# Kernel tuning notes

Hardware: AMD Instinct MI355X
Metric: run time of the kernel (lower is better)

The kernel has to match this reference:

```python
import jax, jax.numpy as jnp
import numpy as np

# hyperparams matching init_kwargs
T_LEN = 1024
T_LATENCY = 7
TB = T_LATENCY + 1          # t_len_block
N_OUT = 1024
BATCH = 32
FS_SCALE = 10.0             # FastSigmoid default scale


@jax.custom_vjp
def fast_sigmoid(x):
    # forward: Heaviside; backward: fast-sigmoid surrogate
    return (x > 0).astype(x.dtype)

def _fs_fwd(x):
    return (x > 0).astype(x.dtype), x

def _fs_bwd(x, g):
    return (g / (FS_SCALE * jnp.abs(x) + 1.0) ** 2,)

fast_sigmoid.defvjp(_fs_fwd, _fs_bwd)


def setup_inputs() -> dict:
    key = jax.random.key(0)
    k1, k2, k3, k4 = jax.random.split(key, 4)
    x = jax.random.normal(k1, (T_LEN, BATCH, N_OUT), dtype=jnp.float32) * 0.6
    # raw params; forward applies the clamp/abs 'properties' of the module
    beta_raw = jax.random.uniform(k2, (N_OUT,), minval=0.7, maxval=0.99, dtype=jnp.float32)
    p_raw = jax.random.uniform(k3, (N_OUT,), minval=0.5, maxval=0.95, dtype=jnp.float32)
    b_raw = jax.random.uniform(k4, (N_OUT,), minval=0.2, maxval=1.0, dtype=jnp.float32)
    return {"x": x, "beta_raw": beta_raw, "p_raw": p_raw, "b_raw": b_raw}


def reference(x, beta_raw, p_raw, b_raw):
    T, B, N = x.shape
    tb = TB
    n_blocks = T // tb  # t_pad == 0 by construction
    dt = x.dtype

    # clamped properties
    beta = jnp.clip(beta_raw, 0.001, 0.999)          # [N]
    p = jnp.clip(jnp.abs(p_raw), 0.0, 0.999)         # [N]
    bb = jnp.clip(jnp.abs(b_raw), 0.001, 1.0)        # [N]

    t_idx = jnp.arange(tb)
    expo = t_idx[:, None] - t_idx[None, :]            # [tb,tb], t - s
    lower = expo >= 0
    # causal decay kernel: beta^(t-s) for s<=t  (grouped conv1d equivalent)
    beta_pow = jnp.where(lower[:, :, None],
                         beta[None, None, :] ** jnp.maximum(expo, 0)[:, :, None].astype(dt),
                         jnp.zeros((), dt))           # [tb,tb,N]
    # phi kernel: weight (t-s+1) for s<=t  (conv2d equivalent)
    phi = jnp.where(lower, (expo + 1).astype(dt), jnp.zeros((), dt))  # [tb,tb]
    p_exp = jnp.arange(1, tb + 1, dtype=dt)           # [tb]
    p_pow = p[None, :] ** p_exp[:, None]              # [tb,N]
    inv_p = 1.0 / p                                   # [N]

    def body(carry, x_slice):
        spikes, z, int_mem, a_kernel = carry          # [tb,B,N],[tb,B,N],[B,N],[tb,B,N]
        sg = jax.lax.stop_gradient(spikes)            # detach_spike_grad=True
        maskf = (jnp.max(sg, axis=0) > 0).astype(dt)  # [B,N] any spike in prev block
        # refractory masking of input
        xs = jnp.where(z < maskf[None], jnp.zeros((), dt), x_slice)
        v_init = int_mem * (1.0 - maskf)
        # adaptation update
        a_at_spike = jnp.sum(a_kernel * sg, axis=0) + inv_p          # [B,N]
        decay_steps = jnp.sum(z > 1, axis=0).astype(dt)              # [B,N]
        new_a = a_at_spike * jnp.power(p[None, :], decay_steps)
        a = a_kernel[-1] * (1.0 - maskf) + new_a * maskf             # [B,N]
        a_k = p_pow[:, None, :] * a[None]                             # [tb,B,N]
        v_th = 1.0 + bb[None, None, :] * a_k                          # [tb,B,N]
        # --- Block forward ---
        cur = xs.at[0].add(beta[None, :] * v_init)
        membrane = jnp.einsum('tsn,sbn->tbn', beta_pow, cur)          # causal decayed sum
        faulty = fast_sigmoid(membrane - v_th)                        # [tb,B,N] 0/1
        z_new = jnp.einsum('ts,sbn->tbn', phi, faulty)
        # g(): keep only entries exactly 1, straight-through grad
        spikes_new = z_new - jax.lax.stop_gradient(
            jnp.where(z_new == 1.0, jnp.zeros((), dt), z_new))
        return (spikes_new, z_new, membrane[-1], a_k), spikes_new

    z0 = jnp.zeros((tb, B, N), dt)
    carry0 = (z0, z0, jnp.zeros((B, N), dt), z0)
    xb = x.reshape(n_blocks, tb, B, N)
    _, out = jax.lax.scan(body, carry0, xb)
    return out.reshape(T, B, N)
```

## Files before the change

### kernel.cpp

```cpp
#include <hip/hip_runtime.h>


constexpr int T_LEN = 1024;
constexpr int TB    = 8;
constexpr int NBLK  = T_LEN / TB;
constexpr int BATCH = 32;
constexpr int NOUT  = 1024;
constexpr int BN    = BATCH * NOUT;
constexpr int PF    = 8;

__global__ __launch_bounds__(64, 1)
void snn_blocks_kernel(const float* __restrict__ x,
                       const float* __restrict__ beta_raw,
                       const float* __restrict__ p_raw,
                       const float* __restrict__ b_raw,
                       float* __restrict__ out)
{
    const int gid = blockIdx.x * 64 + threadIdx.x;
    const int n   = gid & (NOUT - 1);

    double beta = (double)beta_raw[n];
    beta = beta < 0.001 ? 0.001 : (beta > 0.999 ? 0.999 : beta);
    double p = fabs((double)p_raw[n]);
    p = p > 0.999 ? 0.999 : p;
    double bb = fabs((double)b_raw[n]);
    bb = bb < 0.001 ? 0.001 : (bb > 1.0 ? 1.0 : bb);
    const double inv_p = 1.0 / p;

    double ppow[9];
    ppow[0] = 1.0;
#pragma unroll
    for (int i = 1; i <= 8; ++i) ppow[i] = ppow[i - 1] * p;

    double bbp[8];
#pragma unroll
    for (int t = 0; t < 8; ++t) bbp[t] = bb * ppow[t + 1];

    double m = 0.0;
    double a = 0.0;
    int zprev[8];
#pragma unroll
    for (int t = 0; t < 8; ++t) zprev[t] = 0;

    const float* xg = x + gid;
    float*       og = out + gid;

    float xb[PF][8];
#pragma unroll
    for (int k = 0; k < PF; ++k) {
#pragma unroll
        for (int t = 0; t < 8; ++t)
            xb[k][t] = xg[(ptrdiff_t)(k * TB + t) * BN];
    }

#pragma unroll 8
    for (int blk = 0; blk < NBLK; ++blk) {
        const int slot = blk & (PF - 1);
        float cur[8];
#pragma unroll
        for (int t = 0; t < 8; ++t) cur[t] = xb[slot][t];

        const int pfb = blk + PF;
        if (pfb < NBLK) {
#pragma unroll
            for (int t = 0; t < 8; ++t)
                xb[slot][t] = xg[(ptrdiff_t)(pfb * TB + t) * BN];
        }

        int maskf = 0;
        int decay = 0;
        double ssum = 0.0;
#pragma unroll
        for (int t = 0; t < 8; ++t) {
            maskf |= (zprev[t] == 1);
            decay += (zprev[t] > 1) ? 1 : 0;
            ssum  += (zprev[t] == 1) ? ppow[t + 1] : 0.0;
        }

        const double a_at = a * ssum + inv_p;
        double pd = 1.0;
        pd *= (decay & 1) ? p       : 1.0;
        pd *= (decay & 2) ? ppow[2] : 1.0;
        pd *= (decay & 4) ? ppow[4] : 1.0;
        pd *= (decay & 8) ? ppow[8] : 1.0;
        const double new_a = a_at * pd;

        if (maskf) { a = new_a;      m = 0.0; }
        else       { a = ppow[8] * a;          }

        int c = 0, zc = 0;
        float* o = og + (ptrdiff_t)blk * TB * BN;
#pragma unroll
        for (int t = 0; t < 8; ++t) {
            double xv = (double)cur[t];
            if (maskf && zprev[t] == 0) xv = 0.0;
            m = beta * m + xv;
            const double vth = 1.0 + bbp[t] * a;
            const int f = (m - vth > 0.0) ? 1 : 0;
            c  += f;
            zc += c;
            zprev[t] = zc;
            __builtin_nontemporal_store((zc == 1) ? 1.0f : 0.0f,
                                        o + (ptrdiff_t)t * BN);
        }
    }
}

extern "C" void kernel_launch(void* const* d_in, const int* in_sizes, int n_in,
                              void* d_out, int out_size, void* d_ws, size_t ws_size,
                              hipStream_t stream) {
    const float* x        = (const float*)d_in[0];
    const float* beta_raw = (const float*)d_in[1];
    const float* p_raw    = (const float*)d_in[2];
    const float* b_raw    = (const float*)d_in[3];
    float* out            = (float*)d_out;

    dim3 grid(BN / 64);
    dim3 block(64);
    snn_blocks_kernel<<<grid, block, 0, stream>>>(x, beta_raw, p_raw, b_raw, out);
}
```

Measured before the change: 248.6 us.

## Prefetch input blocks via global_load_lds into LDS ring buffer with vmcnt waits

Replaces the register-held 8-block prefetch with direct global-to-LDS async loads into a 5-slot LDS ring, with prefetch depth 4 and explicit s_waitcnt vmcnt throttling. It also precomputes the next block's spike-mask summary (maskf, decay, ssum, zero bitmask) inside the time loop, so the zprev array is no longer kept. The aim is to free VGPRs and keep memory loads in flight without holding them in registers. The hand-tuned vmcnt counts depend on the nontemporal stores also counting toward vmcnt, so a wrong count could cause stale reads or extra stalls.

```diff
diff --git a/kernel.cpp b/kernel.cpp
--- a/kernel.cpp
+++ b/kernel.cpp
@@ -7,7 +7,13 @@
 constexpr int BATCH = 32;
 constexpr int NOUT  = 1024;
 constexpr int BN    = BATCH * NOUT;
-constexpr int PF    = 8;
+constexpr int PF    = 4;
+constexpr int SLOTS = 5;
+
+#define WAITVM(N) asm volatile("s_waitcnt vmcnt(" #N ")" ::: "memory")
+
+typedef const __attribute__((address_space(1))) void* gptr_t;
+typedef __attribute__((address_space(3))) void*       sptr_t;
 
 __global__ __launch_bounds__(64, 1)
 void snn_blocks_kernel(const float* __restrict__ x,
@@ -16,8 +22,11 @@
                        const float* __restrict__ b_raw,
                        float* __restrict__ out)
 {
-    const int gid = blockIdx.x * 64 + threadIdx.x;
-    const int n   = gid & (NOUT - 1);
+    __shared__ float lds[SLOTS][TB][64];
+
+    const int lane = threadIdx.x;
+    const int gid  = blockIdx.x * 64 + lane;
+    const int n    = gid & (NOUT - 1);
 
     double beta = (double)beta_raw[n];
     beta = beta < 0.001 ? 0.001 : (beta > 0.999 ? 0.999 : beta);
@@ -38,44 +47,31 @@
 
     double m = 0.0;
     double a = 0.0;
-    int zprev[8];
-#pragma unroll
-    for (int t = 0; t < 8; ++t) zprev[t] = 0;
+    int    maskf = 0;
+    int    decay = 0;
+    double ssum  = 0.0;
+    int    zzero = 0xFF;
 
     const float* xg = x + gid;
     float*       og = out + gid;
 
-    float xb[PF][8];
 #pragma unroll
     for (int k = 0; k < PF; ++k) {
 #pragma unroll
-        for (int t = 0; t < 8; ++t)
-            xb[k][t] = xg[(ptrdiff_t)(k * TB + t) * BN];
+        for (int t = 0; t < TB; ++t) {
+            __builtin_amdgcn_global_load_lds(
+                (gptr_t)(xg + (ptrdiff_t)(k * TB + t) * BN),
+                (sptr_t)&lds[k][t][0], 4, 0, 0);
+        }
     }
 
-#pragma unroll 8
-    for (int blk = 0; blk < NBLK; ++blk) {
-        const int slot = blk & (PF - 1);
+    int rs = 0;
+    int ws = PF % SLOTS;
+
+    auto body = [&](int blk) {
         float cur[8];
 #pragma unroll
-        for (int t = 0; t < 8; ++t) cur[t] = xb[slot][t];
-
-        const int pfb = blk + PF;
-        if (pfb < NBLK) {
-#pragma unroll
-            for (int t = 0; t < 8; ++t)
-                xb[slot][t] = xg[(ptrdiff_t)(pfb * TB + t) * BN];
-        }
-
-        int maskf = 0;
-        int decay = 0;
-        double ssum = 0.0;
-#pragma unroll
-        for (int t = 0; t < 8; ++t) {
-            maskf |= (zprev[t] == 1);
-            decay += (zprev[t] > 1) ? 1 : 0;
-            ssum  += (zprev[t] == 1) ? ppow[t + 1] : 0.0;
-        }
+        for (int t = 0; t < 8; ++t) cur[t] = lds[rs][t][lane];
 
         const double a_at = a * ssum + inv_p;
         double pd = 1.0;
@@ -85,24 +81,54 @@
         pd *= (decay & 8) ? ppow[8] : 1.0;
         const double new_a = a_at * pd;
 
-        if (maskf) { a = new_a;      m = 0.0; }
-        else       { a = ppow[8] * a;          }
+        if (maskf) { a = new_a;     m = 0.0; }
+        else       { a = ppow[8] * a;        }
 
+        int nmaskf = 0, ndecay = 0, nzzero = 0;
+        double nssum = 0.0;
         int c = 0, zc = 0;
         float* o = og + (ptrdiff_t)blk * TB * BN;
 #pragma unroll
         for (int t = 0; t < 8; ++t) {
             double xv = (double)cur[t];
-            if (maskf && zprev[t] == 0) xv = 0.0;
+            if (maskf && ((zzero >> t) & 1)) xv = 0.0;
             m = beta * m + xv;
             const double vth = 1.0 + bbp[t] * a;
             const int f = (m - vth > 0.0) ? 1 : 0;
             c  += f;
             zc += c;
-            zprev[t] = zc;
+            nmaskf |= (zc == 1);
+            ndecay += (zc > 1) ? 1 : 0;
+            nssum  += (zc == 1) ? ppow[t + 1] : 0.0;
+            nzzero |= (zc == 0) ? (1 << t) : 0;
             __builtin_nontemporal_store((zc == 1) ? 1.0f : 0.0f,
                                         o + (ptrdiff_t)t * BN);
         }
+        maskf = nmaskf; decay = ndecay; ssum = nssum; zzero = nzzero;
+
+        const int pfb = blk + PF;
+        if (pfb < NBLK) {
+#pragma unroll
+            for (int t = 0; t < TB; ++t) {
+                __builtin_amdgcn_global_load_lds(
+                    (gptr_t)(xg + (ptrdiff_t)(pfb * TB + t) * BN),
+                    (sptr_t)&lds[ws][t][0], 4, 0, 0);
+            }
+        }
+        if (++rs == SLOTS) rs = 0;
+        if (++ws == SLOTS) ws = 0;
+    };
+
+    WAITVM(24); body(0);
+    WAITVM(32); body(1);
+    WAITVM(40); body(2);
+    for (int blk = 3; blk < NBLK - PF; ++blk) {
+        WAITVM(48);
+        body(blk);
+    }
+    for (int blk = NBLK - PF; blk < NBLK; ++blk) {
+        WAITVM(16);
+        body(blk);
     }
 }
 
```

Result: no change. 246.5 us (-0.8%).
